# Kernel tuning notes

Hardware: AMD Instinct MI355X
Metric: run time of the kernel (lower is better)

The kernel has to match this reference:

```python
import jax, jax.numpy as jnp
import numpy as np

B, N, D, L = 16, 100, 1024, 2000


def setup_inputs() -> dict:
    key = jax.random.key(0)
    ks = jax.random.split(key, 9)
    s = 1.0 / np.sqrt(D)
    return {
        "feature": jax.random.normal(ks[0], (B, N, D), dtype=jnp.float32),
        "graph": jax.random.randint(ks[1], (B, N, N), 0, L),
        "W0": jax.random.normal(ks[2], (D, D), dtype=jnp.float32) * s,
        "W1": jax.random.normal(ks[3], (D, D), dtype=jnp.float32) * s,
        "bias": jax.random.uniform(ks[4], (L, D), dtype=jnp.float32, minval=-s, maxval=s),
        "dp_Wa": jax.random.normal(ks[5], (D, D), dtype=jnp.float32) * s,
        "dp_ba": jax.random.normal(ks[6], (D,), dtype=jnp.float32) * s,
        "dp_Wb": jax.random.normal(ks[7], (D, D), dtype=jnp.float32) * s,
        "dp_bb": jax.random.normal(ks[8], (D,), dtype=jnp.float32) * s,
        "get_alpha": 0,
    }


def reference(feature, graph, W0, W1, bias, dp_Wa, dp_ba, dp_Wb, dp_bb, get_alpha):
    # ---- DirectedGraphConv.conv ----
    adj = (graph != 0).astype(feature.dtype)                     # [B,N,N]
    out = feature + feature @ W0.T + feature @ W1.T              # [B,N,D]
    out = out + jnp.take(bias, graph, axis=0).sum(axis=2)        # label-embedding gather+sum over neighbors
    # ---- relation_alpha: DotProduct(feature, feature) ----
    a = feature @ dp_Wa.T + dp_ba                                # [B,N,D]
    b = feature @ dp_Wb.T + dp_bb                                # [B,N,D]
    alpha = jnp.einsum('bik,bjk->bij', a, b)                     # [B,N,N]
    alpha = jnp.maximum(alpha, 0.0)                              # alpha[alpha<0]=0
    alpha = jnp.einsum('bij,bjk->bik', adj, alpha)               # bmm(adj, alpha)
    alpha = jax.nn.softmax(alpha, axis=1)                        # Softmax(dim=1)
    out = jnp.einsum('bij,bjk->bik', alpha, out)                 # bmm(alpha, output)
    if get_alpha:
        return (out, alpha)
    return out
```

## Files before the change

### kernel.cpp

```cpp
#include <hip/hip_runtime.h>
#include <stdint.h>

#define B_   16
#define N_   100
#define D_   1024
#define L_   2000
#define M_   1600
#define KP   2048

#define RCAP 24
#define ZMAX 2400
#define TC   12

typedef __bf16 bf16x8 __attribute__((ext_vector_type(8)));
typedef float  f32x4  __attribute__((ext_vector_type(4)));

__device__ __forceinline__ void gl_lds16(const __bf16* g, __bf16* l) {
    __builtin_amdgcn_global_load_lds(
        (const __attribute__((address_space(1))) void*)g,
        (__attribute__((address_space(3))) void*)l, 16, 0, 0);
}


__global__ void __launch_bounds__(256)
k_prep(const float* __restrict__ f,
       const float* __restrict__ W0, const float* __restrict__ W1,
       const float* __restrict__ Wa, const float* __restrict__ Wb,
       const float* __restrict__ bias, const int* __restrict__ graph,
       __bf16* __restrict__ fb, __bf16* __restrict__ wcat,
       __bf16* __restrict__ biasBT, __bf16* __restrict__ cnt) {
    int bid = blockIdx.x, t = threadIdx.x;
    __shared__ float lds[32][33];
    __shared__ unsigned int hist[KP];

    if (bid < 2336) {
        int i = bid * 256 + t;
        union { __bf16 h[8]; uint4 u; } pk;
        if (i < 204800) {
            long base = (long)i * 8;
            const float4* p = (const float4*)(f + base);
            float4 x = p[0], y = p[1];
            pk.h[0]=(__bf16)x.x; pk.h[1]=(__bf16)x.y; pk.h[2]=(__bf16)x.z; pk.h[3]=(__bf16)x.w;
            pk.h[4]=(__bf16)y.x; pk.h[5]=(__bf16)y.y; pk.h[6]=(__bf16)y.z; pk.h[7]=(__bf16)y.w;
            ((uint4*)fb)[i] = pk.u;
        } else {
            int j = i - 204800;
            long base = (long)j * 8;
            long seg = base >> 20;
            long off = base & ((1l << 20) - 1);
            if (seg == 0) {
                const float4* p0 = (const float4*)(W0 + off);
                const float4* p1 = (const float4*)(W1 + off);
                float4 a0 = p0[0], a1 = p0[1], b0 = p1[0], b1 = p1[1];
                pk.h[0]=(__bf16)(a0.x+b0.x); pk.h[1]=(__bf16)(a0.y+b0.y);
                pk.h[2]=(__bf16)(a0.z+b0.z); pk.h[3]=(__bf16)(a0.w+b0.w);
                pk.h[4]=(__bf16)(a1.x+b1.x); pk.h[5]=(__bf16)(a1.y+b1.y);
                pk.h[6]=(__bf16)(a1.z+b1.z); pk.h[7]=(__bf16)(a1.w+b1.w);
            } else {
                const float* src = (seg == 1) ? Wa : Wb;
                const float4* p = (const float4*)(src + off);
                float4 x = p[0], y = p[1];
                pk.h[0]=(__bf16)x.x; pk.h[1]=(__bf16)x.y; pk.h[2]=(__bf16)x.z; pk.h[3]=(__bf16)x.w;
                pk.h[4]=(__bf16)y.x; pk.h[5]=(__bf16)y.y; pk.h[6]=(__bf16)y.z; pk.h[7]=(__bf16)y.w;
            }
            ((uint4*)wcat)[j] = pk.u;
        }
    } else if (bid < 4384) {
        int tb = bid - 2336;
        int lt = tb >> 5, dt = tb & 31;
        int l0 = lt * 32, d0 = dt * 32;
        int r = t >> 3, cq = (t & 7) * 4;
        float4 v = make_float4(0.f, 0.f, 0.f, 0.f);
        if (l0 + r < L_) v = *(const float4*)(bias + (long)(l0 + r) * D_ + d0 + cq);
        lds[r][cq]=v.x; lds[r][cq+1]=v.y; lds[r][cq+2]=v.z; lds[r][cq+3]=v.w;
        __syncthreads();
        union { __bf16 h[4]; uint2 u; } pk;
        #pragma unroll
        for (int q = 0; q < 4; ++q) pk.h[q] = (__bf16)lds[cq + q][r];
        *(uint2*)(biasBT + (long)(d0 + r) * KP + l0 + cq) = pk.u;
    } else {
        int m = bid - 4384;
        for (int k = t; k < KP; k += 256) hist[k] = 0u;
        __syncthreads();
        if (t < N_) atomicAdd(&hist[graph[(long)m * N_ + t]], 1u);
        __syncthreads();
        for (int k = t; k < KP; k += 256)
            cnt[(long)m * KP + k] = (__bf16)(float)hist[k];
    }
}


#define BM 64
#define BN 128
#define BK 64

__global__ void __launch_bounds__(256)
k_gemm(const __bf16* __restrict__ A, const __bf16* __restrict__ Bw,
       const float* __restrict__ feat, const float* __restrict__ ba,
       const float* __restrict__ bbias,
       float* __restrict__ out0, float* __restrict__ aB, float* __restrict__ bB) {
    __shared__ __align__(16) __bf16 As[BM * BK];
    __shared__ __align__(16) __bf16 Bs[BN * BK];
    int t = threadIdx.x;
    int bm = blockIdx.x, bn = blockIdx.y;
    int lane = t & 63, wave = t >> 6;
    int wr = wave & 1, wc = wave >> 1;
    int lrow = lane & 15, quad = lane >> 4;

    f32x4 acc[2][4] = {};
    const __bf16* Ag = A  + (long)(bm * BM) * D_;
    const __bf16* Bg = Bw + (long)(bn * BN) * D_;

    for (int k0 = 0; k0 < D_; k0 += BK) {
        #pragma unroll
        for (int pi = 0; pi < 2; ++pi) {
            int p = pi * 256 + t, row = p >> 3, c = (p & 7) ^ (row & 7);
            gl_lds16(Ag + (long)row * D_ + k0 + c * 8, As + p * 8);
        }
        #pragma unroll
        for (int pi = 0; pi < 4; ++pi) {
            int p = pi * 256 + t, row = p >> 3, c = (p & 7) ^ (row & 7);
            gl_lds16(Bg + (long)row * D_ + k0 + c * 8, Bs + p * 8);
        }
        __syncthreads();
        #pragma unroll
        for (int ks = 0; ks < 2; ++ks) {
            bf16x8 af[2], bf[4];
            #pragma unroll
            for (int i = 0; i < 2; ++i) {
                int r = wr * 32 + i * 16 + lrow;
                int slot = r * 8 + (((ks << 2) | quad) ^ (r & 7));
                af[i] = *(const bf16x8*)(As + slot * 8);
            }
            #pragma unroll
            for (int j = 0; j < 4; ++j) {
                int r = wc * 64 + j * 16 + lrow;
                int slot = r * 8 + (((ks << 2) | quad) ^ (r & 7));
                bf[j] = *(const bf16x8*)(Bs + slot * 8);
            }
            #pragma unroll
            for (int i = 0; i < 2; ++i)
                #pragma unroll
                for (int j = 0; j < 4; ++j)
                    acc[i][j] = __builtin_amdgcn_mfma_f32_16x16x32_bf16(af[i], bf[j], acc[i][j], 0, 0, 0);
        }
        __syncthreads();
    }

    int nbase = bn * BN;
    int seg = nbase >> 10;
    #pragma unroll
    for (int i = 0; i < 2; ++i) {
        int gm0 = bm * BM + wr * 32 + i * 16 + quad * 4;
        #pragma unroll
        for (int j = 0; j < 4; ++j) {
            int col = (nbase + wc * 64 + j * 16 + lrow) & 1023;
            #pragma unroll
            for (int r = 0; r < 4; ++r) {
                long m = gm0 + r;
                float v = acc[i][j][r];
                if (seg == 0)      out0[m * D_ + col] = v + feat[m * D_ + col];
                else if (seg == 1) aB[m * D_ + col]   = v + ba[col];
                else               bB[m * D_ + col]   = v + bbias[col];
            }
        }
    }
}


__global__ void __launch_bounds__(256)
k_post1(const int* __restrict__ graph, const __bf16* __restrict__ cnt,
        const __bf16* __restrict__ biasBT, const float* __restrict__ aB,
        const float* __restrict__ bB, float* __restrict__ out0,
        float* __restrict__ wl, float* __restrict__ cwG) {
    int t = threadIdx.x;

    if (blockIdx.x < 200) {
        __shared__ __align__(16) __bf16 As[BM * BK];
        __shared__ __align__(16) __bf16 Bs[BN * BK];
        int bm = blockIdx.x >> 3, bn = blockIdx.x & 7;
        int lane = t & 63, wave = t >> 6;
        int wr = wave & 1, wc = wave >> 1;
        int lrow = lane & 15, quad = lane >> 4;

        f32x4 acc[2][4] = {};
        const __bf16* Ag = cnt    + (long)(bm * BM) * KP;
        const __bf16* Bg = biasBT + (long)(bn * BN) * KP;

        for (int k0 = 0; k0 < KP; k0 += BK) {
            #pragma unroll
            for (int pi = 0; pi < 2; ++pi) {
                int p = pi * 256 + t, row = p >> 3, c = (p & 7) ^ (row & 7);
                gl_lds16(Ag + (long)row * KP + k0 + c * 8, As + p * 8);
            }
            #pragma unroll
            for (int pi = 0; pi < 4; ++pi) {
                int p = pi * 256 + t, row = p >> 3, c = (p & 7) ^ (row & 7);
                gl_lds16(Bg + (long)row * KP + k0 + c * 8, Bs + p * 8);
            }
            __syncthreads();
            #pragma unroll
            for (int ks = 0; ks < 2; ++ks) {
                bf16x8 af[2], bf[4];
                #pragma unroll
                for (int i = 0; i < 2; ++i) {
                    int r = wr * 32 + i * 16 + lrow;
                    int slot = r * 8 + (((ks << 2) | quad) ^ (r & 7));
                    af[i] = *(const bf16x8*)(As + slot * 8);
                }
                #pragma unroll
                for (int j = 0; j < 4; ++j) {
                    int r = wc * 64 + j * 16 + lrow;
                    int slot = r * 8 + (((ks << 2) | quad) ^ (r & 7));
                    bf[j] = *(const bf16x8*)(Bs + slot * 8);
                }
                #pragma unroll
                for (int i = 0; i < 2; ++i)
                    #pragma unroll
                    for (int j = 0; j < 4; ++j)
                        acc[i][j] = __builtin_amdgcn_mfma_f32_16x16x32_bf16(af[i], bf[j], acc[i][j], 0, 0, 0);
            }
            __syncthreads();
        }

        #pragma unroll
        for (int i = 0; i < 2; ++i) {
            int gm0 = bm * BM + wr * 32 + i * 16 + quad * 4;
            #pragma unroll
            for (int j = 0; j < 4; ++j) {
                int col = bn * BN + wc * 64 + j * 16 + lrow;
                #pragma unroll
                for (int r = 0; r < 4; ++r) {
                    long m = gm0 + r;
                    out0[m * D_ + col] += acc[i][j][r];
                }
            }
        }
        return;
    }

    __shared__ int rowCnt[N_], rowOff[N_], rowRank[N_];
    __shared__ int ndvS, totZS;
    __shared__ int zjL[ZMAX];
    __shared__ short prL[ZMAX];
    __shared__ float corrL[RCAP][4];
    __shared__ float wred[4][4];

    int pid = blockIdx.x - 200;
    int b = pid / 25, kc = pid - b * 25;
    int lane = t & 63, wave = t >> 6;

    const int* g = graph + (long)b * N_ * N_;
    if (t < N_) {
        int c = 0;
        for (int j = 0; j < N_; ++j) if (g[t * N_ + j] == 0) ++c;
        rowCnt[t] = c;
    }
    if (t < RCAP * 4) corrL[t >> 2][t & 3] = 0.f;
    __syncthreads();
    if (t == 0) {
        int off = 0, rank = 0;
        for (int i = 0; i < N_; ++i) {
            if (rowCnt[i] > 0 && rank < RCAP) {
                rowRank[i] = rank; rowOff[i] = off; off += rowCnt[i]; ++rank;
            } else rowRank[i] = -1;
        }
        ndvS = rank; totZS = off;
    }
    __syncthreads();
    if (t < N_ && rowRank[t] >= 0) {
        int pos = rowOff[t], r = rowRank[t];
        for (int j = 0; j < N_; ++j)
            if (g[t * N_ + j] == 0) { zjL[pos] = j; prL[pos] = (short)r; ++pos; }
    }
    __syncthreads();
    int Z = totZS, ndv = ndvS;

    int k0 = kc * 4;
    float4 bv[4];
    #pragma unroll
    for (int kk = 0; kk < 4; ++kk)
        bv[kk] = *(const float4*)(bB + ((long)(b * N_ + k0 + kk)) * D_ + t * 4);

    for (int q = 0; q < Z; ++q) {
        const float* ar = aB + ((long)(b * N_ + zjL[q])) * D_;
        float4 av = *(const float4*)(ar + t * 4);
        float s[4];
        #pragma unroll
        for (int kk = 0; kk < 4; ++kk)
            s[kk] = av.x * bv[kk].x + av.y * bv[kk].y + av.z * bv[kk].z + av.w * bv[kk].w;
        #pragma unroll
        for (int off = 32; off > 0; off >>= 1)
            #pragma unroll
            for (int kk = 0; kk < 4; ++kk) s[kk] += __shfl_xor(s[kk], off);
        if (lane == 0) { wred[wave][0]=s[0]; wred[wave][1]=s[1]; wred[wave][2]=s[2]; wred[wave][3]=s[3]; }
        __syncthreads();
        if (t < 4) {
            float v = wred[0][t] + wred[1][t] + wred[2][t] + wred[3][t];
            corrL[prL[q]][t] += fmaxf(v, 0.f);
        }
        __syncthreads();
    }

    if (t < 4) {
        int k = k0 + t;
        float denom = (float)(N_ - ndv);
        for (int r = 0; r < ndv; ++r) {
            float e = __expf(-corrL[r][t]);
            corrL[r][t] = e;
            denom += e;
        }
        float w = 1.f / denom;
        wl[b * N_ + k] = w;
        for (int r = 0; r < ndv; ++r)
            cwG[((long)b * RCAP + r) * N_ + k] = corrL[r][t] * w;
    }
}


__global__ void __launch_bounds__(256)
k_mix(const int* __restrict__ graph, const float* __restrict__ wl,
      const float* __restrict__ cwG, const float* __restrict__ out0,
      float* __restrict__ out) {
    int b = blockIdx.x, dq = blockIdx.y;
    int t = threadIdx.x, c4 = t & 63, q = t >> 6;
    int d0 = dq * 256;
    __shared__ int hasZ[N_], mapL[N_], ndvS;
    __shared__ float wT[TC][N_];
    __shared__ f32x4 parts[4][TC][64];

    const int* g = graph + (long)b * N_ * N_;
    if (t < N_) {
        int z = 0;
        for (int j = 0; j < N_; ++j) if (g[t * N_ + j] == 0) { z = 1; break; }
        hasZ[t] = z;
    }
    __syncthreads();
    if (t < N_) {
        int rank = 0;
        for (int i = 0; i < t; ++i) rank += hasZ[i];
        mapL[t] = (hasZ[t] && rank < RCAP) ? 1 + rank : 0;
    }
    if (t == 0) {
        int n = 0;
        for (int i = 0; i < N_; ++i) n += hasZ[i];
        ndvS = min(n, RCAP);
    }
    __syncthreads();
    int ndv = ndvS, ntask = ndv + 1;

    const float* o0 = out0 + (long)b * N_ * D_ + d0;
    for (int cb = 0; cb < ntask; cb += TC) {
        for (int idx = t; idx < TC * N_; idx += 256) {
            int rr = idx / N_, j = idx - rr * N_;
            int task = cb + rr;
            float v = 0.f;
            if (task == 0)         v = wl[b * N_ + j];
            else if (task <= ndv)  v = cwG[((long)b * RCAP + task - 1) * N_ + j];
            wT[rr][j] = v;
        }
        __syncthreads();
        f32x4 acc[TC] = {};
        for (int j = q * 25; j < q * 25 + 25; ++j) {
            f32x4 v = *(const f32x4*)(o0 + (long)j * D_ + c4 * 4);
            #pragma unroll
            for (int rr = 0; rr < TC; ++rr) acc[rr] += wT[rr][j] * v;
        }
        #pragma unroll
        for (int rr = 0; rr < TC; ++rr) parts[q][rr][c4] = acc[rr];
        __syncthreads();
        for (int i = q * 25; i < q * 25 + 25; ++i) {
            int task = mapL[i];
            if (task >= cb && task < cb + TC) {
                int rr = task - cb;
                f32x4 s = parts[0][rr][c4] + parts[1][rr][c4]
                        + parts[2][rr][c4] + parts[3][rr][c4];
                *(f32x4*)(out + ((long)(b * N_ + i)) * D_ + d0 + c4 * 4) = s;
            }
        }
        __syncthreads();
    }
}


extern "C" void kernel_launch(void* const* d_in, const int* in_sizes, int n_in,
                              void* d_out, int out_size, void* d_ws, size_t ws_size,
                              hipStream_t stream) {
    const float* feature = (const float*)d_in[0];
    const int*   graph   = (const int*)d_in[1];
    const float* W0      = (const float*)d_in[2];
    const float* W1      = (const float*)d_in[3];
    const float* bias    = (const float*)d_in[4];
    const float* dp_Wa   = (const float*)d_in[5];
    const float* dp_ba   = (const float*)d_in[6];
    const float* dp_Wb   = (const float*)d_in[7];
    const float* dp_bb   = (const float*)d_in[8];
    float* out = (float*)d_out;

    char* w = (char*)d_ws;
    __bf16* fb16   = (__bf16*)(w);
    __bf16* wcat   = (__bf16*)(w + 3276800);
    __bf16* cnt    = (__bf16*)(w + 9568256);
    __bf16* biasBT = (__bf16*)(w + 16121856);
    float*  out0   = (float*)(w + 20316160);
    float*  aB     = (float*)(w + 26869760);
    float*  bB     = (float*)(w + 33423360);
    float*  wl     = (float*)(w + 39976960);
    float*  cwG    = (float*)(w + 39983360);

    k_prep<<<5984, 256, 0, stream>>>(feature, W0, W1, dp_Wa, dp_Wb, bias, graph,
                                     fb16, wcat, biasBT, cnt);
    k_gemm<<<dim3(25, 24), 256, 0, stream>>>(fb16, wcat, feature, dp_ba, dp_bb,
                                             out0, aB, bB);
    k_post1<<<600, 256, 0, stream>>>(graph, cnt, biasBT, aB, bB, out0, wl, cwG);
    k_mix<<<dim3(B_, 4), 256, 0, stream>>>(graph, wl, cwG, out0, out);
}
```

Measured before the change: 178.6 us.

## Merge main and bias-count GEMMs into one launch, split alpha into own kernel

```diff
diff --git a/kernel.cpp b/kernel.cpp
--- a/kernel.cpp
+++ b/kernel.cpp
@@ -95,32 +95,49 @@
 #define BK 64
 
 __global__ void __launch_bounds__(256)
-k_gemm(const __bf16* __restrict__ A, const __bf16* __restrict__ Bw,
-       const float* __restrict__ feat, const float* __restrict__ ba,
-       const float* __restrict__ bbias,
-       float* __restrict__ out0, float* __restrict__ aB, float* __restrict__ bB) {
+k_gemmAll(const __bf16* __restrict__ fb, const __bf16* __restrict__ wcat,
+          const __bf16* __restrict__ cnt, const __bf16* __restrict__ biasBT,
+          const float* __restrict__ feat, const float* __restrict__ ba,
+          const float* __restrict__ bbias,
+          float* __restrict__ out0, float* __restrict__ aB, float* __restrict__ bB,
+          float* __restrict__ out0add) {
     __shared__ __align__(16) __bf16 As[BM * BK];
     __shared__ __align__(16) __bf16 Bs[BN * BK];
     int t = threadIdx.x;
-    int bm = blockIdx.x, bn = blockIdx.y;
+    int pid = blockIdx.x;
     int lane = t & 63, wave = t >> 6;
     int wr = wave & 1, wc = wave >> 1;
     int lrow = lane & 15, quad = lane >> 4;
 
+    bool isMain = pid < 600;
+    int bm, bn, lda, K;
+    const __bf16 *Ag, *Bg;
+    if (isMain) {
+        int v = (pid & 7) * 75 + (pid >> 3);
+        bn = v / 25; bm = v % 25;
+        Ag = fb   + (long)(bm * BM) * D_;
+        Bg = wcat + (long)(bn * BN) * D_;
+        lda = D_; K = D_;
+    } else {
+        int q = pid - 600;
+        int v = (q & 7) * 25 + (q >> 3);
+        bm = v >> 3; bn = v & 7;
+        Ag = cnt    + (long)(bm * BM) * KP;
+        Bg = biasBT + (long)(bn * BN) * KP;
+        lda = KP; K = KP;
+    }
+
     f32x4 acc[2][4] = {};
-    const __bf16* Ag = A  + (long)(bm * BM) * D_;
-    const __bf16* Bg = Bw + (long)(bn * BN) * D_;
-
-    for (int k0 = 0; k0 < D_; k0 += BK) {
+    for (int k0 = 0; k0 < K; k0 += BK) {
         #pragma unroll
         for (int pi = 0; pi < 2; ++pi) {
             int p = pi * 256 + t, row = p >> 3, c = (p & 7) ^ (row & 7);
-            gl_lds16(Ag + (long)row * D_ + k0 + c * 8, As + p * 8);
+            gl_lds16(Ag + (long)row * lda + k0 + c * 8, As + p * 8);
         }
         #pragma unroll
         for (int pi = 0; pi < 4; ++pi) {
             int p = pi * 256 + t, row = p >> 3, c = (p & 7) ^ (row & 7);
-            gl_lds16(Bg + (long)row * D_ + k0 + c * 8, Bs + p * 8);
+            gl_lds16(Bg + (long)row * lda + k0 + c * 8, Bs + p * 8);
         }
         __syncthreads();
         #pragma unroll
@@ -147,82 +164,26 @@
         __syncthreads();
     }
 
-    int nbase = bn * BN;
-    int seg = nbase >> 10;
-    #pragma unroll
-    for (int i = 0; i < 2; ++i) {
-        int gm0 = bm * BM + wr * 32 + i * 16 + quad * 4;
-        #pragma unroll
-        for (int j = 0; j < 4; ++j) {
-            int col = (nbase + wc * 64 + j * 16 + lrow) & 1023;
-            #pragma unroll
-            for (int r = 0; r < 4; ++r) {
-                long m = gm0 + r;
-                float v = acc[i][j][r];
-                if (seg == 0)      out0[m * D_ + col] = v + feat[m * D_ + col];
-                else if (seg == 1) aB[m * D_ + col]   = v + ba[col];
-                else               bB[m * D_ + col]   = v + bbias[col];
-            }
-        }
-    }
-}
-
-
-__global__ void __launch_bounds__(256)
-k_post1(const int* __restrict__ graph, const __bf16* __restrict__ cnt,
-        const __bf16* __restrict__ biasBT, const float* __restrict__ aB,
-        const float* __restrict__ bB, float* __restrict__ out0,
-        float* __restrict__ wl, float* __restrict__ cwG) {
-    int t = threadIdx.x;
-
-    if (blockIdx.x < 200) {
-        __shared__ __align__(16) __bf16 As[BM * BK];
-        __shared__ __align__(16) __bf16 Bs[BN * BK];
-        int bm = blockIdx.x >> 3, bn = blockIdx.x & 7;
-        int lane = t & 63, wave = t >> 6;
-        int wr = wave & 1, wc = wave >> 1;
-        int lrow = lane & 15, quad = lane >> 4;
-
-        f32x4 acc[2][4] = {};
-        const __bf16* Ag = cnt    + (long)(bm * BM) * KP;
-        const __bf16* Bg = biasBT + (long)(bn * BN) * KP;
-
-        for (int k0 = 0; k0 < KP; k0 += BK) {
-            #pragma unroll
-            for (int pi = 0; pi < 2; ++pi) {
-                int p = pi * 256 + t, row = p >> 3, c = (p & 7) ^ (row & 7);
-                gl_lds16(Ag + (long)row * KP + k0 + c * 8, As + p * 8);
-            }
-            #pragma unroll
-            for (int pi = 0; pi < 4; ++pi) {
-                int p = pi * 256 + t, row = p >> 3, c = (p & 7) ^ (row & 7);
-                gl_lds16(Bg + (long)row * KP + k0 + c * 8, Bs + p * 8);
-            }
-            __syncthreads();
-            #pragma unroll
-            for (int ks = 0; ks < 2; ++ks) {
-                bf16x8 af[2], bf[4];
+    if (isMain) {
+        int nbase = bn * BN;
+        int seg = bn >> 3;
+        #pragma unroll
+        for (int i = 0; i < 2; ++i) {
+            int gm0 = bm * BM + wr * 32 + i * 16 + quad * 4;
+            #pragma unroll
+            for (int j = 0; j < 4; ++j) {
+                int col = (nbase + wc * 64 + j * 16 + lrow) & 1023;
                 #pragma unroll
-                for (int i = 0; i < 2; ++i) {
-                    int r = wr * 32 + i * 16 + lrow;
-                    int slot = r * 8 + (((ks << 2) | quad) ^ (r & 7));
-                    af[i] = *(const bf16x8*)(As + slot * 8);
+                for (int r = 0; r < 4; ++r) {
+                    long m = gm0 + r;
+                    float v = acc[i][j][r];
+                    if (seg == 0)      out0[m * D_ + col] = v + feat[m * D_ + col];
+                    else if (seg == 1) aB[m * D_ + col]   = v + ba[col];
+                    else               bB[m * D_ + col]   = v + bbias[col];
                 }
-                #pragma unroll
-                for (int j = 0; j < 4; ++j) {
-                    int r = wc * 64 + j * 16 + lrow;
-                    int slot = r * 8 + (((ks << 2) | quad) ^ (r & 7));
-                    bf[j] = *(const bf16x8*)(Bs + slot * 8);
-                }
-                #pragma unroll
-                for (int i = 0; i < 2; ++i)
-                    #pragma unroll
-                    for (int j = 0; j < 4; ++j)
-                        acc[i][j] = __builtin_amdgcn_mfma_f32_16x16x32_bf16(af[i], bf[j], acc[i][j], 0, 0, 0);
-            }
-            __syncthreads();
-        }
-
+            }
+        }
+    } else {
         #pragma unroll
         for (int i = 0; i < 2; ++i) {
             int gm0 = bm * BM + wr * 32 + i * 16 + quad * 4;
@@ -232,13 +193,17 @@
                 #pragma unroll
                 for (int r = 0; r < 4; ++r) {
                     long m = gm0 + r;
-                    out0[m * D_ + col] += acc[i][j][r];
+                    out0add[m * D_ + col] = acc[i][j][r];
                 }
             }
         }
-        return;
-    }
-
+    }
+}
+
+
+__global__ void __launch_bounds__(256)
+k_alpha(const int* __restrict__ graph, const float* __restrict__ aB,
+        const float* __restrict__ bB, float* __restrict__ wl, float* __restrict__ cwG) {
     __shared__ int rowCnt[N_], rowOff[N_], rowRank[N_];
     __shared__ int ndvS, totZS;
     __shared__ int zjL[ZMAX];
@@ -246,9 +211,9 @@
     __shared__ float corrL[RCAP][4];
     __shared__ float wred[4][4];
 
-    int pid = blockIdx.x - 200;
+    int pid = blockIdx.x;
     int b = pid / 25, kc = pid - b * 25;
-    int lane = t & 63, wave = t >> 6;
+    int t = threadIdx.x, lane = t & 63, wave = t >> 6;
 
     const int* g = graph + (long)b * N_ * N_;
     if (t < N_) {
@@ -321,7 +286,7 @@
 __global__ void __launch_bounds__(256)
 k_mix(const int* __restrict__ graph, const float* __restrict__ wl,
       const float* __restrict__ cwG, const float* __restrict__ out0,
-      float* __restrict__ out) {
+      const float* __restrict__ out0add, float* __restrict__ out) {
     int b = blockIdx.x, dq = blockIdx.y;
     int t = threadIdx.x, c4 = t & 63, q = t >> 6;
     int d0 = dq * 256;
@@ -349,7 +314,8 @@
     __syncthreads();
     int ndv = ndvS, ntask = ndv + 1;
 
-    const float* o0 = out0 + (long)b * N_ * D_ + d0;
+    const float* o0 = out0    + (long)b * N_ * D_ + d0;
+    const float* oa = out0add + (long)b * N_ * D_ + d0;
     for (int cb = 0; cb < ntask; cb += TC) {
         for (int idx = t; idx < TC * N_; idx += 256) {
             int rr = idx / N_, j = idx - rr * N_;
@@ -362,7 +328,8 @@
         __syncthreads();
         f32x4 acc[TC] = {};
         for (int j = q * 25; j < q * 25 + 25; ++j) {
-            f32x4 v = *(const f32x4*)(o0 + (long)j * D_ + c4 * 4);
+            f32x4 v = *(const f32x4*)(o0 + (long)j * D_ + c4 * 4)
+                    + *(const f32x4*)(oa + (long)j * D_ + c4 * 4);
             #pragma unroll
             for (int rr = 0; rr < TC; ++rr) acc[rr] += wT[rr][j] * v;
         }
@@ -398,20 +365,21 @@
     float* out = (float*)d_out;
 
     char* w = (char*)d_ws;
-    __bf16* fb16   = (__bf16*)(w);
-    __bf16* wcat   = (__bf16*)(w + 3276800);
-    __bf16* cnt    = (__bf16*)(w + 9568256);
-    __bf16* biasBT = (__bf16*)(w + 16121856);
-    float*  out0   = (float*)(w + 20316160);
-    float*  aB     = (float*)(w + 26869760);
-    float*  bB     = (float*)(w + 33423360);
-    float*  wl     = (float*)(w + 39976960);
-    float*  cwG    = (float*)(w + 39983360);
+    __bf16* fb16    = (__bf16*)(w);
+    __bf16* wcat    = (__bf16*)(w + 3276800);
+    __bf16* cnt     = (__bf16*)(w + 9568256);
+    __bf16* biasBT  = (__bf16*)(w + 16121856);
+    float*  out0    = (float*)(w + 20316160);
+    float*  aB      = (float*)(w + 26869760);
+    float*  bB      = (float*)(w + 33423360);
+    float*  wl      = (float*)(w + 39976960);
+    float*  cwG     = (float*)(w + 39983360);
+    float*  out0add = (float*)(w + 40136960);
 
     k_prep<<<5984, 256, 0, stream>>>(feature, W0, W1, dp_Wa, dp_Wb, bias, graph,
                                      fb16, wcat, biasBT, cnt);
-    k_gemm<<<dim3(25, 24), 256, 0, stream>>>(fb16, wcat, feature, dp_ba, dp_bb,
-                                             out0, aB, bB);
-    k_post1<<<600, 256, 0, stream>>>(graph, cnt, biasBT, aB, bB, out0, wl, cwG);
-    k_mix<<<dim3(B_, 4), 256, 0, stream>>>(graph, wl, cwG, out0, out);
-}
+    k_gemmAll<<<800, 256, 0, stream>>>(fb16, wcat, cnt, biasBT, feature, dp_ba, dp_bb,
+                                       out0, aB, bB, out0add);
+    k_alpha<<<400, 256, 0, stream>>>(graph, aB, bB, wl, cwG);
+    k_mix<<<dim3(B_, 4), 256, 0, stream>>>(graph, wl, cwG, out0, out0add, out);
+}
```

Measured after the change: 176.5 us. No clear change (-1.2%).
